# Kernel tuning notes

Measured on AMD Instinct MI355X. Metric: run time of the kernel, lower is better.

## Reference

```python
import jax, jax.numpy as jnp
import numpy as np

TEMPERATURE = 0.8
TOP_P = 0.9
NEG_INF = float('-inf')


def _top_k_filter(logits, k):
    # keep only the top-k logits per row; mask the rest to -inf.
    # torch.topk + scatter mask == threshold at the k-th largest value (ties measure-zero for float logits)
    kth = jax.lax.top_k(logits, k)[0][..., -1:]  # [B, 1]
    return jnp.where(logits < kth, NEG_INF, logits)


def _top_p_filter(logits, p):
    # nucleus filtering: sort desc, cumulative softmax mass, drop tail past p (always keep the top token)
    B, V = logits.shape
    order = jnp.argsort(-logits, axis=-1)                       # [B, V] descending order
    sorted_logits = jnp.take_along_axis(logits, order, axis=-1)
    cdf = jnp.cumsum(jax.nn.softmax(sorted_logits, axis=-1), axis=-1)
    remove_sorted = cdf > p
    remove_sorted = jnp.roll(remove_sorted, 1, axis=-1).at[..., 0].set(False)  # shift so first token crossing p is kept
    rows = jnp.arange(B)[:, None]
    remove = jnp.zeros((B, V), dtype=bool).at[rows, order].set(remove_sorted)  # scatter back to original positions
    return jnp.where(remove, NEG_INF, logits)


def _sample_multinomial(probs, key):
    # inverse-CDF sampling: idx = #{cumsum <= r}
    r = jax.random.uniform(key, (probs.shape[0], 1), dtype=probs.dtype)
    cdf = jnp.cumsum(probs, axis=-1)
    return jnp.sum(cdf <= r, axis=-1, keepdims=True)  # [B, 1] int


def setup_inputs() -> dict:
    key = jax.random.key(0)
    logits = jax.random.normal(key, (256, 50257), dtype=jnp.float32) * 4.0
    return {"logits": logits, "top_k": 50}


def reference(logits, top_k):
    logits = logits / TEMPERATURE
    logits = _top_k_filter(logits, top_k)
    logits = _top_p_filter(logits, TOP_P)
    probs = jax.nn.softmax(logits, axis=-1)
    next_ids = _sample_multinomial(probs, jax.random.fold_in(jax.random.key(0), 1))
    return next_ids
```

## Files before the change

### kernel.cpp

```cpp
#include <hip/hip_runtime.h>
#include <stdint.h>


#define BINS     4096
#define S_CHUNKS 8
#define PB       256
#define SEG      256
#define TB       64
#define CAPN     1024
#define SLOTS    (CAPN / TB)
#define WCAP     256
#define TOPP     0.9f
#define TOPT_F   8.0f
#define OK8      0xC1000000u

__device__ __forceinline__ unsigned orderKey(float x) {
  unsigned u = __float_as_uint(x);
  return (u & 0x80000000u) ? ~u : (u | 0x80000000u);
}

__device__ __forceinline__ void threefry2x32(unsigned k0, unsigned k1,
                                             unsigned x0, unsigned x1,
                                             unsigned &o0, unsigned &o1) {
  unsigned k2 = k0 ^ k1 ^ 0x1BD11BDAu;
  x0 += k0; x1 += k1;
#define TFR(rr) { x0 += x1; x1 = (x1 << (rr)) | (x1 >> (32 - (rr))); x1 ^= x0; }
  TFR(13) TFR(15) TFR(26) TFR(6)
  x0 += k1; x1 += k2 + 1u;
  TFR(17) TFR(29) TFR(16) TFR(24)
  x0 += k2; x1 += k0 + 2u;
  TFR(13) TFR(15) TFR(26) TFR(6)
  x0 += k0; x1 += k1 + 3u;
  TFR(17) TFR(29) TFR(16) TFR(24)
  x0 += k1; x1 += k2 + 4u;
  TFR(13) TFR(15) TFR(26) TFR(6)
  x0 += k2; x1 += k0 + 5u;
#undef TFR
  o0 = x0; o1 = x1;
}

__global__ __launch_bounds__(PB) void k_pass1(
    const float* __restrict__ logits, const int* __restrict__ topk_ptr,
    int* __restrict__ scnt, float* __restrict__ svals, int* __restrict__ sidxs,
    int V) {
  __shared__ unsigned hist[BINS];
  __shared__ unsigned psum[PB];
  __shared__ float    lval[SEG];
  __shared__ int      lidx[SEG];
  __shared__ unsigned lcnt, ocnt, s_thr;
  __shared__ int      s_bstar, s_g;

  const int row = blockIdx.y, chunk = blockIdx.x, tid = threadIdx.x;
  const float* __restrict__ rp = logits + (size_t)row * (size_t)V;
  const float4* __restrict__ rp4 = (const float4*)rp;
  const int V4 = V >> 2;
  const int beg = (int)((long long)chunk * V4 / S_CHUNKS);
  const int end = (int)((long long)(chunk + 1) * V4 / S_CHUNKS);
  const bool last = (chunk == S_CHUNKS - 1);
  const int rembeg = V4 << 2;
  const int sb = row * S_CHUNKS + chunk;
  float* __restrict__ ov = svals + (size_t)sb * SEG;
  int*   __restrict__ oi = sidxs + (size_t)sb * SEG;

  if (tid == 0) { lcnt = 0u; ocnt = 0u; }
  __syncthreads();

  for (int i = beg + tid; i < end; i += PB) {
    float4 v = rp4[i];
    float vv[4] = {v.x, v.y, v.z, v.w};
#pragma unroll
    for (int c = 0; c < 4; ++c) {
      if (vv[c] >= TOPT_F) {
        unsigned pos = atomicAdd(&lcnt, 1u);
        if (pos < SEG) { lval[pos] = vv[c]; lidx[pos] = (i << 2) + c; }
      }
    }
  }
  if (last) {
    for (int i = rembeg + tid; i < V; i += PB) {
      float x = rp[i];
      if (x >= TOPT_F) {
        unsigned pos = atomicAdd(&lcnt, 1u);
        if (pos < SEG) { lval[pos] = x; lidx[pos] = i; }
      }
    }
  }
  __syncthreads();

  int k = topk_ptr[0];
  if (k < 1) k = 1;
  if (k > V) k = V;
  const int ec = (end - beg) * 4 + (last ? (V - rembeg) : 0);
  const int keff = (k < ec) ? k : ec;

  const unsigned total = lcnt;
  const bool fast = (total >= (unsigned)keff) && (total <= (unsigned)SEG);

  if (fast) {
    if (tid < 64) {
      unsigned key[SEG / 64];
#pragma unroll
      for (int t = 0; t < SEG / 64; ++t) {
        int i = tid + t * 64;
        key[t] = (i < (int)total) ? orderKey(lval[i]) : 0u;
      }
      unsigned lo = 1u, hi = 0xFFFFFFFFu;
      while (lo < hi) {
        unsigned mid = lo + ((hi - lo + 1u) >> 1);
        int c = 0;
#pragma unroll
        for (int t = 0; t < SEG / 64; ++t)
          c += __popcll(__ballot(key[t] >= mid));
        if (c >= keff) lo = mid; else hi = mid - 1u;
      }
      if (tid == 0) s_thr = (lo >= OK8 + 4u) ? lo - 4u : 0u;
    }
    __syncthreads();
    if (s_thr != 0u) {
      const unsigned thr = s_thr;
      for (int i = tid; i < (int)total; i += PB) {
        float x = lval[i];
        if (orderKey(x) >= thr) {
          unsigned pos = atomicAdd(&ocnt, 1u);
          ov[pos] = x;
          oi[pos] = lidx[i];
        }
      }
      __syncthreads();
      if (tid == 0) scnt[sb] = (int)ocnt;
      return;
    }
  }

  for (int i = tid; i < BINS; i += PB) hist[i] = 0u;
  __syncthreads();
  for (int i = beg + tid; i < end; i += PB) {
    float4 v = rp4[i];
    atomicAdd(&hist[orderKey(v.x) >> 20], 1u);
    atomicAdd(&hist[orderKey(v.y) >> 20], 1u);
    atomicAdd(&hist[orderKey(v.z) >> 20], 1u);
    atomicAdd(&hist[orderKey(v.w) >> 20], 1u);
  }
  if (last)
    for (int i = rembeg + tid; i < V; i += PB)
      atomicAdd(&hist[orderKey(rp[i]) >> 20], 1u);
  __syncthreads();

  const int C = BINS / PB;
  {
    unsigned s = 0;
#pragma unroll
    for (int j = 0; j < C; ++j) s += hist[tid * C + j];
    psum[tid] = s;
  }
  __syncthreads();
  for (int d = 1; d < PB; d <<= 1) {
    unsigned v = psum[tid];
    unsigned w = (tid + d < PB) ? psum[tid + d] : 0u;
    __syncthreads();
    psum[tid] = v + w;
    __syncthreads();
  }
  if (psum[tid] >= (unsigned)keff &&
      (tid == PB - 1 || psum[tid + 1] < (unsigned)keff))
    s_g = tid;
  __syncthreads();
  if (tid == 0) {
    int g = s_g;
    unsigned cum = (g < PB - 1) ? psum[g + 1] : 0u;
    int bstar = g * C;
    for (int b = g * C + C - 1; b >= g * C; --b) {
      cum += hist[b];
      if (cum >= (unsigned)keff) { bstar = b; break; }
    }
    s_bstar = bstar;
  }
  __syncthreads();
  {
    unsigned uk = (unsigned)s_bstar << 20;
    const unsigned ukey = (uk >= 4u) ? uk - 4u : 0u;
    for (int i = beg + tid; i < end; i += PB) {
      float4 v = rp4[i];
      float vv[4] = {v.x, v.y, v.z, v.w};
#pragma unroll
      for (int c = 0; c < 4; ++c) {
        if (orderKey(vv[c]) >= ukey) {
          unsigned pos = atomicAdd(&ocnt, 1u);
          if (pos < SEG) { ov[pos] = vv[c]; oi[pos] = (i << 2) + c; }
        }
      }
    }
    if (last)
      for (int i = rembeg + tid; i < V; i += PB) {
        float x = rp[i];
        if (orderKey(x) >= ukey) {
          unsigned pos = atomicAdd(&ocnt, 1u);
          if (pos < SEG) { ov[pos] = x; oi[pos] = i; }
        }
      }
    __syncthreads();
    if (tid == 0) {
      unsigned t = ocnt;
      scnt[sb] = (int)((t > (unsigned)SEG) ? (unsigned)SEG : t);
    }
  }
}

__global__ __launch_bounds__(TB) void k_tail(
    const int* __restrict__ scnt, const float* __restrict__ svals,
    const int* __restrict__ sidxs, const int* __restrict__ topk_ptr,
    int* __restrict__ out, int V) {
  __shared__ float sval[CAPN];
  __shared__ int   sidx[CAPN];
  __shared__ float wv[WCAP];
  __shared__ int   wi[WCAP];
  __shared__ float ovv[WCAP];
  __shared__ int   oii[WCAP];
  __shared__ float ev[WCAP];
  __shared__ short ord[WCAP];
  __shared__ int   s_off[S_CHUNKS + 1];
  __shared__ unsigned s_wc;
  __shared__ int   s_K;
  __shared__ float s_S2, s_r;

  const int row = blockIdx.x, tid = threadIdx.x;
  int k = topk_ptr[0];
  if (k < 1) k = 1;
  if (k > V) k = V;

  if (tid == 0) {
    int off = 0;
    for (int c = 0; c < S_CHUNKS; ++c) { s_off[c] = off; off += scnt[row * S_CHUNKS + c]; }
    s_off[S_CHUNKS] = off;
    s_wc = 0u;
  }
  __syncthreads();
  int n = s_off[S_CHUNKS];
  if (n > CAPN) n = CAPN;
  if (n == 0) { if (tid == 0) out[row] = V; return; }

  for (int c = 0; c < S_CHUNKS; ++c) {
    int o = s_off[c];
    if (o >= CAPN) break;
    int cn = s_off[c + 1] - o;
    if (o + cn > CAPN) cn = CAPN - o;
    const float* __restrict__ gv = svals + (size_t)(row * S_CHUNKS + c) * SEG;
    const int*   __restrict__ gi = sidxs + (size_t)(row * S_CHUNKS + c) * SEG;
    for (int i = tid; i < cn; i += TB) {
      sval[o + i] = gv[i] / 0.8f;
      sidx[o + i] = gi[i];
    }
  }
  __syncthreads();

  unsigned key[SLOTS];
#pragma unroll
  for (int t = 0; t < SLOTS; ++t) {
    int i = tid + t * TB;
    key[t] = (i < n) ? orderKey(sval[i]) : 0u;
  }

  const int kk = (k < n) ? k : n;
  unsigned lo = 1u, hi = 0xFFFFFFFFu;
  while (lo < hi) {
    unsigned mid = lo + ((hi - lo + 1u) >> 1);
    int c = 0;
#pragma unroll
    for (int t = 0; t < SLOTS; ++t)
      c += __popcll(__ballot(key[t] >= mid));
    if (c >= kk) lo = mid; else hi = mid - 1u;
  }
  const unsigned kv = lo;

#pragma unroll
  for (int t = 0; t < SLOTS; ++t) {
    int i = tid + t * TB;
    if (i < n && key[t] >= kv) {
      unsigned pos = atomicAdd(&s_wc, 1u);
      if (pos < WCAP) { wv[pos] = sval[i]; wi[pos] = sidx[i]; }
    }
  }
  __syncthreads();
  int ns = (int)s_wc;
  if (ns > WCAP) ns = WCAP;

  for (int i = tid; i < ns; i += TB) {
    float v = wv[i];
    int   id = wi[i];
    int   rk = 0;
    for (int j = 0; j < ns; ++j) {
      float vj = wv[j];
      rk += (vj > v) || (vj == v && wi[j] < id);
    }
    ovv[rk] = v;
    oii[rk] = id;
  }
  __syncthreads();

  const float mx = ovv[0];
  for (int i = tid; i < ns; i += TB) ev[i] = expf(ovv[i] - mx);
  __syncthreads();

  if (tid == 0) {
    float S = 0.f;
    for (int i = 0; i < ns; ++i) S += ev[i];
    float c = 0.f;
    int K = ns;
    for (int i = 0; i < ns; ++i) {
      if (i > 0 && c > TOPP) { K = i; break; }
      c += ev[i] / S;
    }
    float S2 = 0.f;
    for (int i = 0; i < K; ++i) S2 += ev[i];
    s_K = K;
    s_S2 = S2;

    unsigned kk0, kk1, o0, o1;
    threefry2x32(0u, 0u, 0u, 1u, kk0, kk1);
    threefry2x32(kk0, kk1, 0u, (unsigned)row, o0, o1);
    unsigned bits = o0 ^ o1;
    float r = __uint_as_float((bits >> 9) | 0x3F800000u) - 1.0f;
    s_r = (r < 0.f) ? 0.f : r;
  }
  __syncthreads();
  const int K = s_K;

  for (int i = tid; i < K; i += TB) {
    int id = oii[i];
    int rk = 0;
    for (int j = 0; j < K; ++j) rk += (oii[j] < id);
    ord[rk] = (short)i;
  }
  __syncthreads();

  if (tid == 0) {
    const float S2 = s_S2;
    const float rr = s_r;
    float c = 0.f;
    int ans = V;
    for (int t = 0; t < K; ++t) {
      int i = ord[t];
      c += ev[i] / S2;
      if (c > rr) { ans = oii[i]; break; }
    }
    out[row] = ans;
  }
}

extern "C" void kernel_launch(void* const* d_in, const int* in_sizes, int n_in,
                              void* d_out, int out_size, void* d_ws, size_t ws_size,
                              hipStream_t stream) {
  const float* logits = (const float*)d_in[0];
  const int*   topk   = (const int*)d_in[1];
  int*         out    = (int*)d_out;
  const int B = out_size;
  const int V = in_sizes[0] / B;

  char* ws = (char*)d_ws;
  int*   scnt  = (int*)ws;
  float* svals = (float*)(ws + (size_t)B * S_CHUNKS * 4);
  int*   sidxs = (int*)(ws + (size_t)B * S_CHUNKS * 4 +
                        (size_t)B * S_CHUNKS * SEG * 4);

  hipLaunchKernelGGL(k_pass1, dim3(S_CHUNKS, B), dim3(PB), 0, stream,
                     logits, topk, scnt, svals, sidxs, V);
  hipLaunchKernelGGL(k_tail, dim3(B), dim3(TB), 0, stream,
                     scnt, svals, sidxs, topk, out, V);
}
```

Before: 112.5 us.

## Drop per-chunk histogram path, defer rare fallback to per-row tail rescan

```diff
diff --git a/kernel.cpp b/kernel.cpp
--- a/kernel.cpp
+++ b/kernel.cpp
@@ -2,8 +2,7 @@
 #include <stdint.h>
 
 
-#define BINS     4096
-#define S_CHUNKS 8
+#define S_CHUNKS 16
 #define PB       256
 #define SEG      256
 #define TB       64
@@ -17,6 +16,10 @@
 __device__ __forceinline__ unsigned orderKey(float x) {
   unsigned u = __float_as_uint(x);
   return (u & 0x80000000u) ? ~u : (u | 0x80000000u);
+}
+__device__ __forceinline__ float unorderKey(unsigned k) {
+  unsigned u = (k & 0x80000000u) ? (k & 0x7FFFFFFFu) : ~k;
+  return __uint_as_float(u);
 }
 
 __device__ __forceinline__ void threefry2x32(unsigned k0, unsigned k1,
@@ -43,12 +46,9 @@
     const float* __restrict__ logits, const int* __restrict__ topk_ptr,
     int* __restrict__ scnt, float* __restrict__ svals, int* __restrict__ sidxs,
     int V) {
-  __shared__ unsigned hist[BINS];
-  __shared__ unsigned psum[PB];
   __shared__ float    lval[SEG];
   __shared__ int      lidx[SEG];
   __shared__ unsigned lcnt, ocnt, s_thr;
-  __shared__ int      s_bstar, s_g;
 
   const int row = blockIdx.y, chunk = blockIdx.x, tid = threadIdx.x;
   const float* __restrict__ rp = logits + (size_t)row * (size_t)V;
@@ -59,32 +59,42 @@
   const bool last = (chunk == S_CHUNKS - 1);
   const int rembeg = V4 << 2;
   const int sb = row * S_CHUNKS + chunk;
-  float* __restrict__ ov = svals + (size_t)sb * SEG;
-  int*   __restrict__ oi = sidxs + (size_t)sb * SEG;
 
   if (tid == 0) { lcnt = 0u; ocnt = 0u; }
   __syncthreads();
 
-  for (int i = beg + tid; i < end; i += PB) {
-    float4 v = rp4[i];
-    float vv[4] = {v.x, v.y, v.z, v.w};
-#pragma unroll
-    for (int c = 0; c < 4; ++c) {
-      if (vv[c] >= TOPT_F) {
-        unsigned pos = atomicAdd(&lcnt, 1u);
-        if (pos < SEG) { lval[pos] = vv[c]; lidx[pos] = (i << 2) + c; }
-      }
-    }
-  }
-  if (last) {
-    for (int i = rembeg + tid; i < V; i += PB) {
-      float x = rp[i];
-      if (x >= TOPT_F) {
-        unsigned pos = atomicAdd(&lcnt, 1u);
-        if (pos < SEG) { lval[pos] = x; lidx[pos] = i; }
-      }
-    }
-  }
+#define PROC(x, idx) do {                                   \
+    float _v = (x);                                         \
+    if (_v >= TOPT_F) {                                     \
+      unsigned _p = atomicAdd(&lcnt, 1u);                   \
+      if (_p < SEG) { lval[_p] = _v; lidx[_p] = (idx); }    \
+    } } while (0)
+
+  for (int i = beg + tid; i < end; i += 4 * PB) {
+    const int e1 = end - 1;
+    const int i1 = i + PB, i2 = i + 2 * PB, i3 = i + 3 * PB;
+    float4 v0 = rp4[i];
+    float4 v1 = rp4[i1 < end ? i1 : e1];
+    float4 v2 = rp4[i2 < end ? i2 : e1];
+    float4 v3 = rp4[i3 < end ? i3 : e1];
+    PROC(v0.x, (i << 2)); PROC(v0.y, (i << 2) + 1);
+    PROC(v0.z, (i << 2) + 2); PROC(v0.w, (i << 2) + 3);
+    if (i1 < end) {
+      PROC(v1.x, (i1 << 2)); PROC(v1.y, (i1 << 2) + 1);
+      PROC(v1.z, (i1 << 2) + 2); PROC(v1.w, (i1 << 2) + 3);
+    }
+    if (i2 < end) {
+      PROC(v2.x, (i2 << 2)); PROC(v2.y, (i2 << 2) + 1);
+      PROC(v2.z, (i2 << 2) + 2); PROC(v2.w, (i2 << 2) + 3);
+    }
+    if (i3 < end) {
+      PROC(v3.x, (i3 << 2)); PROC(v3.y, (i3 << 2) + 1);
+      PROC(v3.z, (i3 << 2) + 2); PROC(v3.w, (i3 << 2) + 3);
+    }
+  }
+  if (last)
+    for (int i = rembeg + tid; i < V; i += PB) PROC(rp[i], i);
+#undef PROC
   __syncthreads();
 
   int k = topk_ptr[0];
@@ -94,9 +104,12 @@
   const int keff = (k < ec) ? k : ec;
 
   const unsigned total = lcnt;
-  const bool fast = (total >= (unsigned)keff) && (total <= (unsigned)SEG);
-
-  if (fast) {
+  if (total > (unsigned)SEG) {
+    if (tid == 0) scnt[sb] = -1;
+    return;
+  }
+
+  if ((int)total >= keff) {
     if (tid < 64) {
       unsigned key[SEG / 64];
 #pragma unroll
@@ -113,103 +126,52 @@
           c += __popcll(__ballot(key[t] >= mid));
         if (c >= keff) lo = mid; else hi = mid - 1u;
       }
-      if (tid == 0) s_thr = (lo >= OK8 + 4u) ? lo - 4u : 0u;
-    }
-    __syncthreads();
-    if (s_thr != 0u) {
-      const unsigned thr = s_thr;
-      for (int i = tid; i < (int)total; i += PB) {
-        float x = lval[i];
-        if (orderKey(x) >= thr) {
-          unsigned pos = atomicAdd(&ocnt, 1u);
-          ov[pos] = x;
-          oi[pos] = lidx[i];
-        }
-      }
-      __syncthreads();
-      if (tid == 0) scnt[sb] = (int)ocnt;
-      return;
-    }
-  }
-
-  for (int i = tid; i < BINS; i += PB) hist[i] = 0u;
-  __syncthreads();
-  for (int i = beg + tid; i < end; i += PB) {
-    float4 v = rp4[i];
-    atomicAdd(&hist[orderKey(v.x) >> 20], 1u);
-    atomicAdd(&hist[orderKey(v.y) >> 20], 1u);
-    atomicAdd(&hist[orderKey(v.z) >> 20], 1u);
-    atomicAdd(&hist[orderKey(v.w) >> 20], 1u);
-  }
-  if (last)
-    for (int i = rembeg + tid; i < V; i += PB)
-      atomicAdd(&hist[orderKey(rp[i]) >> 20], 1u);
-  __syncthreads();
-
-  const int C = BINS / PB;
-  {
-    unsigned s = 0;
-#pragma unroll
-    for (int j = 0; j < C; ++j) s += hist[tid * C + j];
-    psum[tid] = s;
-  }
-  __syncthreads();
-  for (int d = 1; d < PB; d <<= 1) {
-    unsigned v = psum[tid];
-    unsigned w = (tid + d < PB) ? psum[tid + d] : 0u;
-    __syncthreads();
-    psum[tid] = v + w;
-    __syncthreads();
-  }
-  if (psum[tid] >= (unsigned)keff &&
-      (tid == PB - 1 || psum[tid + 1] < (unsigned)keff))
-    s_g = tid;
-  __syncthreads();
-  if (tid == 0) {
-    int g = s_g;
-    unsigned cum = (g < PB - 1) ? psum[g + 1] : 0u;
-    int bstar = g * C;
-    for (int b = g * C + C - 1; b >= g * C; --b) {
-      cum += hist[b];
-      if (cum >= (unsigned)keff) { bstar = b; break; }
-    }
-    s_bstar = bstar;
-  }
-  __syncthreads();
-  {
-    unsigned uk = (unsigned)s_bstar << 20;
-    const unsigned ukey = (uk >= 4u) ? uk - 4u : 0u;
-    for (int i = beg + tid; i < end; i += PB) {
-      float4 v = rp4[i];
-      float vv[4] = {v.x, v.y, v.z, v.w};
-#pragma unroll
-      for (int c = 0; c < 4; ++c) {
-        if (orderKey(vv[c]) >= ukey) {
-          unsigned pos = atomicAdd(&ocnt, 1u);
-          if (pos < SEG) { ov[pos] = vv[c]; oi[pos] = (i << 2) + c; }
-        }
-      }
-    }
-    if (last)
-      for (int i = rembeg + tid; i < V; i += PB) {
-        float x = rp[i];
-        if (orderKey(x) >= ukey) {
-          unsigned pos = atomicAdd(&ocnt, 1u);
-          if (pos < SEG) { ov[pos] = x; oi[pos] = i; }
-        }
-      }
-    __syncthreads();
-    if (tid == 0) {
-      unsigned t = ocnt;
-      scnt[sb] = (int)((t > (unsigned)SEG) ? (unsigned)SEG : t);
-    }
-  }
+      if (tid == 0) s_thr = (lo >= OK8 + 4u) ? lo - 4u : OK8;
+    }
+  } else {
+    if (tid == 0) s_thr = OK8;
+  }
+  __syncthreads();
+
+  const unsigned thr = s_thr;
+  float* __restrict__ ov = svals + (size_t)sb * SEG;
+  int*   __restrict__ oi = sidxs + (size_t)sb * SEG;
+  for (int i = tid; i < (int)total; i += PB) {
+    float x = lval[i];
+    if (orderKey(x) >= thr) {
+      unsigned pos = atomicAdd(&ocnt, 1u);
+      ov[pos] = x;
+      oi[pos] = lidx[i];
+    }
+  }
+  __syncthreads();
+  if (tid == 0) scnt[sb] = (int)ocnt;
+}
+
+__device__ __forceinline__ unsigned kth_key(const float* sval, int n, int kk,
+                                            int tid) {
+  unsigned key[SLOTS];
+#pragma unroll
+  for (int t = 0; t < SLOTS; ++t) {
+    int i = tid + t * TB;
+    key[t] = (i < n) ? orderKey(sval[i]) : 0u;
+  }
+  unsigned lo = 1u, hi = 0xFFFFFFFFu;
+  while (lo < hi) {
+    unsigned mid = lo + ((hi - lo + 1u) >> 1);
+    int c = 0;
+#pragma unroll
+    for (int t = 0; t < SLOTS; ++t)
+      c += __popcll(__ballot(key[t] >= mid));
+    if (c >= kk) lo = mid; else hi = mid - 1u;
+  }
+  return lo;
 }
 
 __global__ __launch_bounds__(TB) void k_tail(
-    const int* __restrict__ scnt, const float* __restrict__ svals,
-    const int* __restrict__ sidxs, const int* __restrict__ topk_ptr,
-    int* __restrict__ out, int V) {
+    const float* __restrict__ logits, const int* __restrict__ scnt,
+    const float* __restrict__ svals, const int* __restrict__ sidxs,
+    const int* __restrict__ topk_ptr, int* __restrict__ out, int V) {
   __shared__ float sval[CAPN];
   __shared__ int   sidx[CAPN];
   __shared__ float wv[WCAP];
@@ -218,64 +180,84 @@
   __shared__ int   oii[WCAP];
   __shared__ float ev[WCAP];
   __shared__ short ord[WCAP];
-  __shared__ int   s_off[S_CHUNKS + 1];
-  __shared__ unsigned s_wc;
+  __shared__ unsigned s_wc, s_sc;
   __shared__ int   s_K;
   __shared__ float s_S2, s_r;
 
   const int row = blockIdx.x, tid = threadIdx.x;
+  const float* __restrict__ rp = logits + (size_t)row * (size_t)V;
   int k = topk_ptr[0];
   if (k < 1) k = 1;
   if (k > V) k = V;
 
-  if (tid == 0) {
-    int off = 0;
-    for (int c = 0; c < S_CHUNKS; ++c) { s_off[c] = off; off += scnt[row * S_CHUNKS + c]; }
-    s_off[S_CHUNKS] = off;
-    s_wc = 0u;
-  }
-  __syncthreads();
-  int n = s_off[S_CHUNKS];
-  if (n > CAPN) n = CAPN;
-  if (n == 0) { if (tid == 0) out[row] = V; return; }
-
-  for (int c = 0; c < S_CHUNKS; ++c) {
-    int o = s_off[c];
-    if (o >= CAPN) break;
-    int cn = s_off[c + 1] - o;
-    if (o + cn > CAPN) cn = CAPN - o;
-    const float* __restrict__ gv = svals + (size_t)(row * S_CHUNKS + c) * SEG;
-    const int*   __restrict__ gi = sidxs + (size_t)(row * S_CHUNKS + c) * SEG;
-    for (int i = tid; i < cn; i += TB) {
-      sval[o + i] = gv[i] / 0.8f;
-      sidx[o + i] = gi[i];
-    }
-  }
-  __syncthreads();
-
-  unsigned key[SLOTS];
+  if (tid == 0) { s_wc = 0u; s_sc = 0u; }
+  __syncthreads();
+
+  bool slow = false;
+  int n = 0;
+  {
+    int off[S_CHUNKS + 1];
+    off[0] = 0;
+    for (int c = 0; c < S_CHUNKS; ++c) {
+      int cc = scnt[row * S_CHUNKS + c];
+      if (cc < 0) { slow = true; cc = 0; }
+      off[c + 1] = off[c] + cc;
+    }
+    n = off[S_CHUNKS];
+    if (n > CAPN) slow = true;
+    if (!slow) {
+      for (int c = 0; c < S_CHUNKS; ++c) {
+        const int o = off[c], cn = off[c + 1] - o;
+        const float* __restrict__ gv = svals + (size_t)(row * S_CHUNKS + c) * SEG;
+        const int*   __restrict__ gi = sidxs + (size_t)(row * S_CHUNKS + c) * SEG;
+        for (int i = tid; i < cn; i += TB) {
+          sval[o + i] = gv[i] / 0.8f;
+          sidx[o + i] = gi[i];
+        }
+      }
+    }
+  }
+  __syncthreads();
+
+  unsigned kvs = 0u;
+  int kk = 0;
+  if (!slow && n > 0) {
+    kk = (k < n) ? k : n;
+    kvs = kth_key(sval, n, kk, tid);
+    if (unorderKey(kvs) < 10.01f) slow = true;
+  }
+  if (n == 0 && !slow) { if (tid == 0) out[row] = V; return; }
+
+  if (slow) {
+    const int kr = (k < V) ? k : V;
+    unsigned lo = 1u, hi = 0xFFFFFFFFu;
+    while (lo < hi) {
+      unsigned mid = lo + ((hi - lo + 1u) >> 1);
+      int c = 0;
+      for (int i = tid; i < V; i += TB) c += (orderKey(rp[i]) >= mid);
+      for (int off = 32; off; off >>= 1) c += __shfl_down(c, off);
+      c = __shfl(c, 0);
+      if (c >= kr) lo = mid; else hi = mid - 1u;
+    }
+    const unsigned thr = (lo >= 5u) ? lo - 4u : 1u;
+    for (int i = tid; i < V; i += TB) {
+      float x = rp[i];
+      if (orderKey(x) >= thr) {
+        unsigned pos = atomicAdd(&s_sc, 1u);
+        if (pos < CAPN) { sval[pos] = x / 0.8f; sidx[pos] = i; }
+      }
+    }
+    __syncthreads();
+    n = (int)s_sc;
+    if (n > CAPN) n = CAPN;
+    kk = (k < n) ? k : n;
+    kvs = kth_key(sval, n, kk, tid);
+  }
+
 #pragma unroll
   for (int t = 0; t < SLOTS; ++t) {
     int i = tid + t * TB;
-    key[t] = (i < n) ? orderKey(sval[i]) : 0u;
-  }
-
-  const int kk = (k < n) ? k : n;
-  unsigned lo = 1u, hi = 0xFFFFFFFFu;
-  while (lo < hi) {
-    unsigned mid = lo + ((hi - lo + 1u) >> 1);
-    int c = 0;
-#pragma unroll
-    for (int t = 0; t < SLOTS; ++t)
-      c += __popcll(__ballot(key[t] >= mid));
-    if (c >= kk) lo = mid; else hi = mid - 1u;
-  }
-  const unsigned kv = lo;
-
-#pragma unroll
-  for (int t = 0; t < SLOTS; ++t) {
-    int i = tid + t * TB;
-    if (i < n && key[t] >= kv) {
+    if (i < n && orderKey(sval[i]) >= kvs) {
       unsigned pos = atomicAdd(&s_wc, 1u);
       if (pos < WCAP) { wv[pos] = sval[i]; wi[pos] = sidx[i]; }
     }
@@ -365,5 +347,5 @@
   hipLaunchKernelGGL(k_pass1, dim3(S_CHUNKS, B), dim3(PB), 0, stream,
                      logits, topk, scnt, svals, sidxs, V);
   hipLaunchKernelGGL(k_tail, dim3(B), dim3(TB), 0, stream,
-                     scnt, svals, sidxs, topk, out, V);
-}
+                     logits, scnt, svals, sidxs, topk, out, V);
+}
```

Result: slower. 118.8 us (+5.5%).
